# Kernel tuning notes

Hardware: AMD Instinct MI355X
Metric: run time of the kernel (lower is better)

The kernel has to match this reference:

```python
import jax, jax.numpy as jnp
import numpy as np

N = 50000
E = 800000
D_IN = 128
D_HID = 128
NUM_LAYERS = 3


def setup_inputs() -> dict:
    key = jax.random.key(0)
    ks = jax.random.split(key, 8)
    x = jax.random.normal(ks[0], (N, D_IN), dtype=jnp.float32)
    edge_index = jax.random.randint(ks[1], (2, E), 0, N, dtype=jnp.int64)
    edge_weight = jnp.ones((E,), dtype=jnp.float32)
    # GCNConv params: glorot-ish weights [in, out], zero bias
    def w(k, fi, fo):
        return jax.random.normal(k, (fi, fo), dtype=jnp.float32) * (1.0 / np.sqrt(fi))
    W0 = w(ks[2], D_IN, D_HID)
    b0 = jnp.zeros((D_HID,), dtype=jnp.float32)
    W1 = w(ks[3], D_HID, D_HID)
    b1 = jnp.zeros((D_HID,), dtype=jnp.float32)
    W2 = w(ks[4], D_HID, D_HID)
    b2 = jnp.zeros((D_HID,), dtype=jnp.float32)
    return {"x": x, "edge_index": edge_index, "edge_weight": edge_weight,
            "W0": W0, "b0": b0, "W1": W1, "b1": b1, "W2": W2, "b2": b2}


def _gcn_layer(h, src, dst, norm, W, b, n):
    # linear transform then degree-normalized scatter-add aggregation
    h = h @ W                                   # [N, d_out]
    msg = h[src] * norm[:, None]                # gather + scale, [E+N, d_out]
    out = jax.ops.segment_sum(msg, dst, num_segments=n)  # scatter-add
    return out + b


def reference(x, edge_index, edge_weight, W0, b0, W1, b1, W2, b2):
    n = x.shape[0]
    loop = jnp.arange(n, dtype=edge_index.dtype)
    src = jnp.concatenate([edge_index[0], loop])   # add self-loops (fill=1)
    dst = jnp.concatenate([edge_index[1], loop])
    ew = jnp.concatenate([edge_weight, jnp.ones((n,), dtype=edge_weight.dtype)])
    # symmetric normalization: deg computed on target (col), norm = d^-1/2[src]*w*d^-1/2[dst]
    deg = jax.ops.segment_sum(ew, dst, num_segments=n)
    dis = jnp.where(deg > 0, jax.lax.rsqrt(deg), 0.0)
    norm = dis[src] * ew * dis[dst]               # [E+N]
    z = x
    for (W, b) in ((W0, b0), (W1, b1), (W2, b2)):
        z = _gcn_layer(z, src, dst, norm, W, b, n)
        z = jax.nn.relu(z)
    return z
```

## Files before the change

kernel.cpp:

```cpp
#include <hip/hip_runtime.h>

#define D 128
#define NB 250
#define BN 200
#define NBLK 512
#define CAP 7168
#define PADB 600

typedef float f2v __attribute__((ext_vector_type(2)));
typedef short bf16x8 __attribute__((ext_vector_type(8)));
typedef float f32x4 __attribute__((ext_vector_type(4)));

__device__ __forceinline__ unsigned bf16r(float f) {
  unsigned u = __float_as_uint(f);
  return (u + 0x7fffu + ((u >> 16) & 1u)) >> 16;
}


__global__ __launch_bounds__(256) void k_pre1(const int* __restrict__ dst, int* __restrict__ M, int E,
                                              const float* __restrict__ X, unsigned short* __restrict__ Xb,
                                              int total4, int GC,
                                              const float* __restrict__ W0, const float* __restrict__ W1,
                                              const float* __restrict__ W2, unsigned short* __restrict__ Wt) {
  __shared__ int lh[NB];
  int b = blockIdx.x;
  int tid = threadIdx.x;
  if (b < NBLK) {
    for (int i = tid; i < NB; i += 256) lh[i] = 0;
    __syncthreads();
    const int EPB = (E + NBLK - 1) / NBLK;
    int e0 = b * EPB;
    int e1 = min(e0 + EPB, E);
    for (int e = e0 + tid; e < e1; e += 256) atomicAdd(&lh[dst[e] / BN], 1);
    __syncthreads();
    for (int i = tid; i < NB; i += 256) M[i * NBLK + b] = lh[i];
  } else if (b < NBLK + GC) {
    int i = (b - NBLK) * 256 + tid;
    if (i < total4) {
      float4 v = ((const float4*)X)[i];
      ushort4 o;
      o.x = (unsigned short)bf16r(v.x);
      o.y = (unsigned short)bf16r(v.y);
      o.z = (unsigned short)bf16r(v.z);
      o.w = (unsigned short)bf16r(v.w);
      ((ushort4*)Xb)[i] = o;
    }
  } else {
    int i = (b - NBLK - GC) * 256 + tid;
    if (i < 3 * 16384) {
      int l = i >> 14;
      int r = i & 16383;
      int nn = r >> 7, kk = r & 127;
      const float* W = (l == 0) ? W0 : (l == 1) ? W1 : W2;
      Wt[i] = (unsigned short)bf16r(W[kk * 128 + nn]);
    }
  }
}


__global__ __launch_bounds__(256) void k_blocksum(const int* __restrict__ cnt, int* __restrict__ bsum, int n) {
  int i = blockIdx.x * 256 + threadIdx.x;
  int v = (i < n) ? cnt[i] : 0;
#pragma unroll
  for (int off = 32; off > 0; off >>= 1) v += __shfl_down(v, off);
  __shared__ int ws[4];
  if ((threadIdx.x & 63) == 0) ws[threadIdx.x >> 6] = v;
  __syncthreads();
  if (threadIdx.x == 0) bsum[blockIdx.x] = ws[0] + ws[1] + ws[2] + ws[3];
}

__global__ __launch_bounds__(512) void k_scanb2(const int* __restrict__ bsum, int* __restrict__ boff, int nb) {
  __shared__ int s[512];
  int t = threadIdx.x;
  int v = (t < nb) ? bsum[t] : 0;
  s[t] = v;
  __syncthreads();
#pragma unroll
  for (int off = 1; off < 512; off <<= 1) {
    int u = (t >= off) ? s[t - off] : 0;
    __syncthreads();
    s[t] += u;
    __syncthreads();
  }
  if (t < nb) boff[t] = s[t] - v;
}

__global__ __launch_bounds__(256) void k_scanm(int* __restrict__ M, const int* __restrict__ boff,
                                               int* __restrict__ bbase, int flatN, int Etot) {
  __shared__ int s[256];
  int t = threadIdx.x;
  int i = blockIdx.x * 256 + t;
  int v = (i < flatN) ? M[i] : 0;
  s[t] = v;
  __syncthreads();
#pragma unroll
  for (int off = 1; off < 256; off <<= 1) {
    int u = (t >= off) ? s[t - off] : 0;
    __syncthreads();
    s[t] += u;
    __syncthreads();
  }
  int ex = s[t] - v + boff[blockIdx.x];
  if (i < flatN) {
    M[i] = ex;
    if ((i & (NBLK - 1)) == 0) bbase[i / NBLK] = ex;
  }
  if (i == 0) bbase[NB] = Etot;
}


__global__ __launch_bounds__(256) void k_pre2(const unsigned short* __restrict__ Zb,
                                              const unsigned short* __restrict__ Wt,
                                              unsigned short* __restrict__ H, int n, int GG,
                                              const int* __restrict__ src, const int* __restrict__ dst,
                                              const float* __restrict__ ew, const int* __restrict__ M,
                                              uint2* __restrict__ part, int E) {
  __shared__ int lcur[NB];
  int b = blockIdx.x;
  if (b < GG) {
    int lane = threadIdx.x & 63;
    int wid  = threadIdx.x >> 6;
    int row0 = b * 16;
    int r  = lane & 15;
    int kg = lane >> 4;
    int c0 = wid * 32;
    const size_t abase  = (size_t)(row0 + r) * 128 + kg * 8;
    const size_t b0base = (size_t)(c0 + r) * 128 + kg * 8;
    const size_t b1base = (size_t)(c0 + 16 + r) * 128 + kg * 8;
    f32x4 acc0 = {0.f, 0.f, 0.f, 0.f};
    f32x4 acc1 = {0.f, 0.f, 0.f, 0.f};
#pragma unroll
    for (int k0 = 0; k0 < 128; k0 += 32) {
      bf16x8 a  = *(const bf16x8*)&Zb[abase + k0];
      bf16x8 b0 = *(const bf16x8*)&Wt[b0base + k0];
      bf16x8 b1 = *(const bf16x8*)&Wt[b1base + k0];
      acc0 = __builtin_amdgcn_mfma_f32_16x16x32_bf16(a, b0, acc0, 0, 0, 0);
      acc1 = __builtin_amdgcn_mfma_f32_16x16x32_bf16(a, b1, acc1, 0, 0, 0);
    }
    int orow = row0 + kg * 4;
#pragma unroll
    for (int j = 0; j < 4; ++j) {
      H[(size_t)(orow + j) * 128 + c0 + r]      = (unsigned short)bf16r(acc0[j]);
      H[(size_t)(orow + j) * 128 + c0 + 16 + r] = (unsigned short)bf16r(acc1[j]);
    }
  } else {
    int blk = b - GG;
    int tid = threadIdx.x;
    for (int i = tid; i < NB; i += 256) lcur[i] = M[i * NBLK + blk];
    __syncthreads();
    const int EPB = (E + NBLK - 1) / NBLK;
    int e0 = blk * EPB;
    int e1 = min(e0 + EPB, E);
    for (int e = e0 + tid; e < e1; e += 256) {
      int d = dst[e];
      int bkt = d / BN;
      int dlow = d - bkt * BN;
      int p = atomicAdd(&lcur[bkt], 1);
      uint2 rec;
      rec.x = (unsigned)src[e] | ((unsigned)dlow << 24);
      rec.y = __float_as_uint(ew[e]);
      part[p] = rec;
    }
  }
}


__global__ __launch_bounds__(256) void k_deg(const uint2* __restrict__ part, const int* __restrict__ bbase,
                                             float* __restrict__ dis, int n) {
  __shared__ float ldeg[BN];
  int b = blockIdx.x;
  int tid = threadIdx.x;
  int base = bbase[b];
  int cnt = bbase[b + 1] - base;
  for (int i = tid; i < BN; i += 256) ldeg[i] = 0.f;
  __syncthreads();
  for (int i = tid; i < cnt; i += 256) {
    uint2 r = part[base + i];
    atomicAdd(&ldeg[r.x >> 24], __uint_as_float(r.y));
  }
  __syncthreads();
  for (int t = tid; t < BN; t += 256) dis[b * BN + t] = rsqrtf(1.0f + ldeg[t]);
}


__global__ __launch_bounds__(256) void k_bsort(const uint2* __restrict__ part, const int* __restrict__ bbase,
                                               const float* __restrict__ dis, unsigned* __restrict__ csr4,
                                               int* __restrict__ rowptr, int n, int Etot) {
  __shared__ uint2 stage[CAP];
  __shared__ int lh[BN];
  __shared__ int s[256];
  int b = blockIdx.x;
  int tid = threadIdx.x;
  int base = bbase[b];
  int cnt = bbase[b + 1] - base;
  int R  = ((base + 3) & ~3) + b * PADB;
  int Rn = ((bbase[b + 1] + 3) & ~3) + (b + 1) * PADB;
  for (int i = tid; i < BN; i += 256) lh[i] = 0;
  __syncthreads();
  for (int i = tid; i < cnt; i += 256) {
    uint2 r = part[base + i];
    if (i < CAP) stage[i] = r;
    atomicAdd(&lh[r.x >> 24], 1);
  }
  __syncthreads();
  int c = (tid < BN) ? lh[tid] : 0;
  int pc = (c + 3) & ~3;
  s[tid] = pc;
  __syncthreads();
#pragma unroll
  for (int off = 1; off < 256; off <<= 1) {
    int u = (tid >= off) ? s[tid - off] : 0;
    __syncthreads();
    s[tid] += u;
    __syncthreads();
  }
  int ex = s[tid] - pc;
  if (tid < BN) {
    lh[tid] = ex;
    rowptr[b * BN + tid] = R + ex;
  }
  if (b == 0 && tid == 0) rowptr[n] = ((Etot + 3) & ~3) + NB * PADB;
  __syncthreads();
  int len = Rn - R;
  for (int i = tid; i < len; i += 256) csr4[R + i] = 0u;
  __syncthreads();
  for (int i = tid; i < cnt; i += 256) {
    uint2 r = (i < CAP) ? stage[i] : part[base + i];
    int dlow = r.x >> 24;
    unsigned srcv = r.x & 0x00FFFFFFu;
    float w = __uint_as_float(r.y) * dis[srcv];
    int p = atomicAdd(&lh[dlow], 1);
    csr4[R + p] = srcv | (bf16r(w) << 16);
  }
}


__global__ __launch_bounds__(256) void k_gemm(const unsigned short* __restrict__ Zb,
                                              const unsigned short* __restrict__ Wt,
                                              unsigned short* __restrict__ H, int n) {
  int lane = threadIdx.x & 63;
  int wid  = threadIdx.x >> 6;
  int row0 = blockIdx.x * 16;
  int r  = lane & 15;
  int kg = lane >> 4;
  int c0 = wid * 32;
  const size_t abase  = (size_t)(row0 + r) * 128 + kg * 8;
  const size_t b0base = (size_t)(c0 + r) * 128 + kg * 8;
  const size_t b1base = (size_t)(c0 + 16 + r) * 128 + kg * 8;
  f32x4 acc0 = {0.f, 0.f, 0.f, 0.f};
  f32x4 acc1 = {0.f, 0.f, 0.f, 0.f};
#pragma unroll
  for (int k0 = 0; k0 < 128; k0 += 32) {
    bf16x8 a  = *(const bf16x8*)&Zb[abase + k0];
    bf16x8 b0 = *(const bf16x8*)&Wt[b0base + k0];
    bf16x8 b1 = *(const bf16x8*)&Wt[b1base + k0];
    acc0 = __builtin_amdgcn_mfma_f32_16x16x32_bf16(a, b0, acc0, 0, 0, 0);
    acc1 = __builtin_amdgcn_mfma_f32_16x16x32_bf16(a, b1, acc1, 0, 0, 0);
  }
  int orow = row0 + kg * 4;
#pragma unroll
  for (int j = 0; j < 4; ++j) {
    H[(size_t)(orow + j) * 128 + c0 + r]      = (unsigned short)bf16r(acc0[j]);
    H[(size_t)(orow + j) * 128 + c0 + 16 + r] = (unsigned short)bf16r(acc1[j]);
  }
}


__global__ __launch_bounds__(256) void k_agg(const unsigned* __restrict__ Hb, const int* __restrict__ rowptr,
                                             const unsigned* __restrict__ csr4, const float* __restrict__ dis,
                                             const float* __restrict__ bias, unsigned* __restrict__ outb,
                                             float* __restrict__ outf, int n) {
  int node = __builtin_amdgcn_readfirstlane(blockIdx.x * 4 + (threadIdx.x >> 6));
  if (node >= n) return;
  int lane = threadIdx.x & 63;
  float ax0 = 0.f, ay0 = 0.f, ax1 = 0.f, ay1 = 0.f;
  int e = rowptr[node];
  const int end = rowptr[node + 1];
  for (; e < end; e += 4) {
    unsigned r0 = __builtin_nontemporal_load(&csr4[e]);
    unsigned r1 = __builtin_nontemporal_load(&csr4[e + 1]);
    unsigned r2 = __builtin_nontemporal_load(&csr4[e + 2]);
    unsigned r3 = __builtin_nontemporal_load(&csr4[e + 3]);
    unsigned s0 = r0 & 0xFFFFu; float w0 = __uint_as_float(r0 & 0xFFFF0000u);
    unsigned s1 = r1 & 0xFFFFu; float w1 = __uint_as_float(r1 & 0xFFFF0000u);
    unsigned s2 = r2 & 0xFFFFu; float w2 = __uint_as_float(r2 & 0xFFFF0000u);
    unsigned s3 = r3 & 0xFFFFu; float w3 = __uint_as_float(r3 & 0xFFFF0000u);
    unsigned g0 = Hb[(size_t)s0 * 64 + lane];
    unsigned g1 = Hb[(size_t)s1 * 64 + lane];
    unsigned g2 = Hb[(size_t)s2 * 64 + lane];
    unsigned g3 = Hb[(size_t)s3 * 64 + lane];
    ax0 = fmaf(__uint_as_float(g0 << 16), w0, ax0); ay0 = fmaf(__uint_as_float(g0 & 0xffff0000u), w0, ay0);
    ax1 = fmaf(__uint_as_float(g1 << 16), w1, ax1); ay1 = fmaf(__uint_as_float(g1 & 0xffff0000u), w1, ay1);
    ax0 = fmaf(__uint_as_float(g2 << 16), w2, ax0); ay0 = fmaf(__uint_as_float(g2 & 0xffff0000u), w2, ay0);
    ax1 = fmaf(__uint_as_float(g3 << 16), w3, ax1); ay1 = fmaf(__uint_as_float(g3 & 0xffff0000u), w3, ay1);
  }
  float ax = ax0 + ax1, ay = ay0 + ay1;
  float dn = dis[node];
  float sn = dn * dn;
  unsigned hv = Hb[(size_t)node * 64 + lane];
  float hvx = __uint_as_float(hv << 16);
  float hvy = __uint_as_float(hv & 0xffff0000u);
  float2 bv = ((const float2*)bias)[lane];
  float ox = fmaxf(fmaf(dn, ax, fmaf(sn, hvx, bv.x)), 0.f);
  float oy = fmaxf(fmaf(dn, ay, fmaf(sn, hvy, bv.y)), 0.f);
  if (outb) {
    outb[(size_t)node * 64 + lane] = bf16r(ox) | (bf16r(oy) << 16);
  } else {
    f2v o; o.x = ox; o.y = oy;
    __builtin_nontemporal_store(o, (f2v*)outf + (size_t)node * 64 + lane);
  }
}


extern "C" void kernel_launch(void* const* d_in, const int* in_sizes, int n_in,
                              void* d_out, int out_size, void* d_ws, size_t ws_size,
                              hipStream_t stream) {
  const float* x  = (const float*)d_in[0];
  const int*   ei = (const int*)d_in[1];
  const float* ew = (const float*)d_in[2];
  const float* W0 = (const float*)d_in[3];
  const float* W1 = (const float*)d_in[5];
  const float* W2 = (const float*)d_in[7];
  const float* bl[3] = {(const float*)d_in[4], (const float*)d_in[6], (const float*)d_in[8]};

  const int n = in_sizes[0] / D;
  const int E = in_sizes[1] / 2;
  const int* src = ei;
  const int* dst = ei + E;

  char* p = (char*)d_ws;
  unsigned short* Zb     = (unsigned short*)p; p += (size_t)n * D * 2;
  unsigned short* H      = (unsigned short*)p; p += (size_t)n * D * 2;
  float*          dis    = (float*)p;          p += (size_t)n * 4;
  int*            rowptr = (int*)p;            p += (size_t)(n + 1) * 4;
  int*            M      = (int*)p;            p += (size_t)NB * NBLK * 4;
  int*            bbase  = (int*)p;            p += (size_t)(NB + 1) * 4;
  int*            bsum2  = (int*)p;            p += 512 * 4;
  int*            boff2  = (int*)p;            p += 512 * 4;
  uint2*          part   = (uint2*)p;          p += (size_t)E * 8;
  unsigned*       csr4   = (unsigned*)p;       p += ((size_t)E + NB * PADB + 64) * 4;
  unsigned short* Wt     = (unsigned short*)p; p += 3 * 16384 * 2;
  (void)ws_size; (void)n_in;

  const int total4 = n * D / 4;
  const int GC = (total4 + 255) / 256;
  const int GW = (3 * 16384 + 255) / 256;
  const int GG = n / 16;
  const int flatN = NB * NBLK;
  const int GS = flatN / 256;

  k_pre1<<<NBLK + GC + GW, 256, 0, stream>>>(dst, M, E, x, Zb, total4, GC, W0, W1, W2, Wt);
  k_blocksum<<<GS, 256, 0, stream>>>(M, bsum2, flatN);
  k_scanb2<<<1, 512, 0, stream>>>(bsum2, boff2, GS);
  k_scanm<<<GS, 256, 0, stream>>>(M, boff2, bbase, flatN, E);
  k_pre2<<<GG + NBLK, 256, 0, stream>>>(Zb, Wt, H, n, GG, src, dst, ew, M, part, E);
  k_deg<<<NB, 256, 0, stream>>>(part, bbase, dis, n);
  k_bsort<<<NB, 256, 0, stream>>>(part, bbase, dis, csr4, rowptr, n, E);

  float* outp = (float*)d_out;
  k_agg<<<(n + 3) / 4, 256, 0, stream>>>((const unsigned*)H, rowptr, csr4, dis, bl[0], (unsigned*)Zb, outp, n);
  for (int l = 1; l < 3; ++l) {
    k_gemm<<<GG, 256, 0, stream>>>(Zb, Wt + l * 16384, H, n);
    unsigned* ob = (l == 2) ? nullptr : (unsigned*)Zb;
    k_agg<<<(n + 3) / 4, 256, 0, stream>>>((const unsigned*)H, rowptr, csr4, dis, bl[l], ob, outp, n);
  }
}
```

Before: 244.9 us.

## Split aggregation across column tiles with edge-parallel lane groups and fp32 CSR

The aggregation kernel now runs on a 2D grid: each wave handles one node and a 16-column slice of the feature row. Its four 16-lane groups process different edges in parallel and are reduced with cross-lane shuffles. The CSR drops the padded 4-aligned packed bf16-weight format for unpadded uint2 entries holding the source index and an fp32 weight, which removes the padding and its zero-fill. This gives more parallelism for low-degree rows and exact weights. In exchange it reads twice the CSR bytes, reads the CSR once per column tile, and uses only 64-byte gathers per row segment.

```diff
diff --git a/kernel.cpp b/kernel.cpp
--- a/kernel.cpp
+++ b/kernel.cpp
@@ -5,7 +5,7 @@
 #define BN 200
 #define NBLK 512
 #define CAP 7168
-#define PADB 600
+#define NT 4
 
 typedef float f2v __attribute__((ext_vector_type(2)));
 typedef short bf16x8 __attribute__((ext_vector_type(8)));
@@ -184,8 +184,8 @@
 
 
 __global__ __launch_bounds__(256) void k_bsort(const uint2* __restrict__ part, const int* __restrict__ bbase,
-                                               const float* __restrict__ dis, unsigned* __restrict__ csr4,
-                                               int* __restrict__ rowptr, int n, int Etot) {
+                                               const float* __restrict__ dis, uint2* __restrict__ csr,
+                                               int* __restrict__ rowptr, int n, int E) {
   __shared__ uint2 stage[CAP];
   __shared__ int lh[BN];
   __shared__ int s[256];
@@ -193,8 +193,6 @@
   int tid = threadIdx.x;
   int base = bbase[b];
   int cnt = bbase[b + 1] - base;
-  int R  = ((base + 3) & ~3) + b * PADB;
-  int Rn = ((bbase[b + 1] + 3) & ~3) + (b + 1) * PADB;
   for (int i = tid; i < BN; i += 256) lh[i] = 0;
   __syncthreads();
   for (int i = tid; i < cnt; i += 256) {
@@ -203,9 +201,8 @@
     atomicAdd(&lh[r.x >> 24], 1);
   }
   __syncthreads();
-  int c = (tid < BN) ? lh[tid] : 0;
-  int pc = (c + 3) & ~3;
-  s[tid] = pc;
+  int v = (tid < BN) ? lh[tid] : 0;
+  s[tid] = v;
   __syncthreads();
 #pragma unroll
   for (int off = 1; off < 256; off <<= 1) {
@@ -214,15 +211,12 @@
     s[tid] += u;
     __syncthreads();
   }
-  int ex = s[tid] - pc;
+  int ex = s[tid] - v;
   if (tid < BN) {
     lh[tid] = ex;
-    rowptr[b * BN + tid] = R + ex;
-  }
-  if (b == 0 && tid == 0) rowptr[n] = ((Etot + 3) & ~3) + NB * PADB;
-  __syncthreads();
-  int len = Rn - R;
-  for (int i = tid; i < len; i += 256) csr4[R + i] = 0u;
+    rowptr[b * BN + tid] = base + ex;
+  }
+  if (b == 0 && tid == 0) rowptr[n] = E;
   __syncthreads();
   for (int i = tid; i < cnt; i += 256) {
     uint2 r = (i < CAP) ? stage[i] : part[base + i];
@@ -230,7 +224,10 @@
     unsigned srcv = r.x & 0x00FFFFFFu;
     float w = __uint_as_float(r.y) * dis[srcv];
     int p = atomicAdd(&lh[dlow], 1);
-    csr4[R + p] = srcv | (bf16r(w) << 16);
+    uint2 o;
+    o.x = srcv;
+    o.y = __float_as_uint(w);
+    csr[base + p] = o;
   }
 }
 
@@ -267,47 +264,49 @@
 
 
 __global__ __launch_bounds__(256) void k_agg(const unsigned* __restrict__ Hb, const int* __restrict__ rowptr,
-                                             const unsigned* __restrict__ csr4, const float* __restrict__ dis,
+                                             const f2v* __restrict__ csr, const float* __restrict__ dis,
                                              const float* __restrict__ bias, unsigned* __restrict__ outb,
                                              float* __restrict__ outf, int n) {
   int node = __builtin_amdgcn_readfirstlane(blockIdx.x * 4 + (threadIdx.x >> 6));
   if (node >= n) return;
   int lane = threadIdx.x & 63;
+  int g = lane >> 4;
+  int col = (blockIdx.y << 4) + (lane & 15);
   float ax0 = 0.f, ay0 = 0.f, ax1 = 0.f, ay1 = 0.f;
   int e = rowptr[node];
   const int end = rowptr[node + 1];
-  for (; e < end; e += 4) {
-    unsigned r0 = __builtin_nontemporal_load(&csr4[e]);
-    unsigned r1 = __builtin_nontemporal_load(&csr4[e + 1]);
-    unsigned r2 = __builtin_nontemporal_load(&csr4[e + 2]);
-    unsigned r3 = __builtin_nontemporal_load(&csr4[e + 3]);
-    unsigned s0 = r0 & 0xFFFFu; float w0 = __uint_as_float(r0 & 0xFFFF0000u);
-    unsigned s1 = r1 & 0xFFFFu; float w1 = __uint_as_float(r1 & 0xFFFF0000u);
-    unsigned s2 = r2 & 0xFFFFu; float w2 = __uint_as_float(r2 & 0xFFFF0000u);
-    unsigned s3 = r3 & 0xFFFFu; float w3 = __uint_as_float(r3 & 0xFFFF0000u);
-    unsigned g0 = Hb[(size_t)s0 * 64 + lane];
-    unsigned g1 = Hb[(size_t)s1 * 64 + lane];
-    unsigned g2 = Hb[(size_t)s2 * 64 + lane];
-    unsigned g3 = Hb[(size_t)s3 * 64 + lane];
+  const int last = end - 1;
+  for (; e < end; e += 8) {
+    int e0 = e + g, e1 = e + 4 + g;
+    f2v r0 = __builtin_nontemporal_load(&csr[min(e0, last)]);
+    f2v r1 = __builtin_nontemporal_load(&csr[min(e1, last)]);
+    int s0 = __float_as_int(r0.x);
+    int s1 = __float_as_int(r1.x);
+    float w0 = (e0 < end) ? r0.y : 0.f;
+    float w1 = (e1 < end) ? r1.y : 0.f;
+    unsigned g0 = Hb[(size_t)s0 * 64 + col];
+    unsigned g1 = Hb[(size_t)s1 * 64 + col];
     ax0 = fmaf(__uint_as_float(g0 << 16), w0, ax0); ay0 = fmaf(__uint_as_float(g0 & 0xffff0000u), w0, ay0);
     ax1 = fmaf(__uint_as_float(g1 << 16), w1, ax1); ay1 = fmaf(__uint_as_float(g1 & 0xffff0000u), w1, ay1);
-    ax0 = fmaf(__uint_as_float(g2 << 16), w2, ax0); ay0 = fmaf(__uint_as_float(g2 & 0xffff0000u), w2, ay0);
-    ax1 = fmaf(__uint_as_float(g3 << 16), w3, ax1); ay1 = fmaf(__uint_as_float(g3 & 0xffff0000u), w3, ay1);
   }
   float ax = ax0 + ax1, ay = ay0 + ay1;
+  ax += __shfl_xor(ax, 16); ay += __shfl_xor(ay, 16);
+  ax += __shfl_xor(ax, 32); ay += __shfl_xor(ay, 32);
   float dn = dis[node];
   float sn = dn * dn;
-  unsigned hv = Hb[(size_t)node * 64 + lane];
+  unsigned hv = Hb[(size_t)node * 64 + col];
   float hvx = __uint_as_float(hv << 16);
   float hvy = __uint_as_float(hv & 0xffff0000u);
-  float2 bv = ((const float2*)bias)[lane];
+  float2 bv = ((const float2*)bias)[col];
   float ox = fmaxf(fmaf(dn, ax, fmaf(sn, hvx, bv.x)), 0.f);
   float oy = fmaxf(fmaf(dn, ay, fmaf(sn, hvy, bv.y)), 0.f);
-  if (outb) {
-    outb[(size_t)node * 64 + lane] = bf16r(ox) | (bf16r(oy) << 16);
-  } else {
-    f2v o; o.x = ox; o.y = oy;
-    __builtin_nontemporal_store(o, (f2v*)outf + (size_t)node * 64 + lane);
+  if (lane < 16) {
+    if (outb) {
+      outb[(size_t)node * 64 + col] = bf16r(ox) | (bf16r(oy) << 16);
+    } else {
+      f2v o; o.x = ox; o.y = oy;
+      __builtin_nontemporal_store(o, (f2v*)outf + (size_t)node * 64 + col);
+    }
   }
 }
 
@@ -338,7 +337,7 @@
   int*            bsum2  = (int*)p;            p += 512 * 4;
   int*            boff2  = (int*)p;            p += 512 * 4;
   uint2*          part   = (uint2*)p;          p += (size_t)E * 8;
-  unsigned*       csr4   = (unsigned*)p;       p += ((size_t)E + NB * PADB + 64) * 4;
+  uint2*          csr    = (uint2*)p;          p += (size_t)E * 8;
   unsigned short* Wt     = (unsigned short*)p; p += 3 * 16384 * 2;
   (void)ws_size; (void)n_in;
 
@@ -355,13 +354,14 @@
   k_scanm<<<GS, 256, 0, stream>>>(M, boff2, bbase, flatN, E);
   k_pre2<<<GG + NBLK, 256, 0, stream>>>(Zb, Wt, H, n, GG, src, dst, ew, M, part, E);
   k_deg<<<NB, 256, 0, stream>>>(part, bbase, dis, n);
-  k_bsort<<<NB, 256, 0, stream>>>(part, bbase, dis, csr4, rowptr, n, E);
+  k_bsort<<<NB, 256, 0, stream>>>(part, bbase, dis, csr, rowptr, n, E);
 
   float* outp = (float*)d_out;
-  k_agg<<<(n + 3) / 4, 256, 0, stream>>>((const unsigned*)H, rowptr, csr4, dis, bl[0], (unsigned*)Zb, outp, n);
+  dim3 agrid((n + 3) / 4, NT);
+  k_agg<<<agrid, 256, 0, stream>>>((const unsigned*)H, rowptr, (const f2v*)csr, dis, bl[0], (unsigned*)Zb, outp, n);
   for (int l = 1; l < 3; ++l) {
     k_gemm<<<GG, 256, 0, stream>>>(Zb, Wt + l * 16384, H, n);
     unsigned* ob = (l == 2) ? nullptr : (unsigned*)Zb;
-    k_agg<<<(n + 3) / 4, 256, 0, stream>>>((const unsigned*)H, rowptr, csr4, dis, bl[l], ob, outp, n);
-  }
-}
+    k_agg<<<agrid, 256, 0, stream>>>((const unsigned*)H, rowptr, (const f2v*)csr, dis, bl[l], ob, outp, n);
+  }
+}
```

Result: slower. 403.1 us (+64.6%).
